# Optimization experiments

Measured on AMD Instinct MI355X. Metric: run time of the kernel, lower is better.

The kernel has to match this reference:

```python
import jax, jax.numpy as jnp
import numpy as np

N = 100000
E = 1600000
DIM_H = 128
NUM_HEADS = 8
HEAD_DIM = DIM_H // NUM_HEADS


def setup_inputs() -> dict:
    key = jax.random.key(0)
    ks = jax.random.split(key, 8)
    s = 1.0 / np.sqrt(DIM_H)
    return {
        "q": jax.random.normal(ks[0], (N, DIM_H), dtype=jnp.float32),
        "kv": jax.random.normal(ks[1], (N, DIM_H), dtype=jnp.float32),
        "edge_index": jax.random.randint(ks[2], (2, E), 0, N, dtype=jnp.int32),
        "W_k": jax.random.normal(ks[3], (DIM_H, DIM_H), dtype=jnp.float32) * s,
        "b_k": jnp.zeros((DIM_H,), dtype=jnp.float32),
        "W_v": jax.random.normal(ks[4], (DIM_H, DIM_H), dtype=jnp.float32) * s,
        "b_v": jnp.zeros((DIM_H,), dtype=jnp.float32),
        "W_o": jax.random.normal(ks[5], (DIM_H, DIM_H), dtype=jnp.float32) * s,
        "b_o": jnp.zeros((DIM_H,), dtype=jnp.float32),
    }


def reference(q, kv, edge_index, W_k, b_k, W_v, b_v, W_o, b_o):
    src, dst = edge_index[0], edge_index[1]
    # Projections: torch Linear is x @ W.T + b
    K = (kv @ W_k.T + b_k).reshape(N, NUM_HEADS, HEAD_DIM)
    V = (kv @ W_v.T + b_v).reshape(N, NUM_HEADS, HEAD_DIM)
    Q = q.reshape(N, NUM_HEADS, HEAD_DIM)

    # Edge-wise attention scores: [E, H]
    scores = jnp.sum(K[src] * Q[dst], axis=-1) / np.sqrt(HEAD_DIM)

    # Sparse softmax over incoming edges of each destination node
    seg_max = jax.ops.segment_max(scores, dst, num_segments=N)  # [N, H]
    ex = jnp.exp(scores - seg_max[dst])
    seg_sum = jax.ops.segment_sum(ex, dst, num_segments=N)  # [N, H]
    attn = ex / (seg_sum[dst] + 1e-16)  # [E, H]

    # Weighted message aggregation (dropout p=0.0 in eval -> identity)
    messages = V[src] * attn[:, :, None]  # [E, H, Hd]
    out = jax.ops.segment_sum(messages, dst, num_segments=N)  # [N, H, Hd]
    out = out.reshape(N, DIM_H)
    return out @ W_o.T + b_o
```

## Files before the change

### kernel.cpp

```cpp
#include <hip/hip_runtime.h>
#include <hip/hip_bf16.h>

#define N_NODES 100000
#define N_EDGES 1600000
#define DIM 128
#define NHEAD 8
#define HDIM 16

#define BSHIFT 9
#define BSZ 512
#define NB 196
#define S1_EDGES 4096

typedef __attribute__((ext_vector_type(8))) short short8;
typedef __attribute__((ext_vector_type(4))) float f32x4;

__device__ __forceinline__ unsigned short f2bf(float f) {
  union { __hip_bfloat16 h; unsigned short u; } c;
  c.h = __float2bfloat16(f);
  return c.u;
}

__global__ __launch_bounds__(256) void cvt3_kernel(const float* __restrict__ a,
                                                   const float* __restrict__ b,
                                                   const float* __restrict__ c,
                                                   unsigned short* __restrict__ y) {
  int i = blockIdx.x * 256 + threadIdx.x;
  const float* src = (i < 4096) ? a : ((i < 8192) ? b : c);
  int j = (i < 4096) ? i : ((i < 8192) ? i - 4096 : i - 8192);
  float4 v = ((const float4*)src)[j];
  ushort4 o;
  o.x = f2bf(v.x); o.y = f2bf(v.y); o.z = f2bf(v.z); o.w = f2bf(v.w);
  ((ushort4*)y)[i] = o;
}


__global__ __launch_bounds__(512) void bhist_kernel(const int* __restrict__ dst,
                                                    int* __restrict__ bcnt) {
  __shared__ int cnt[NB];
  int t = threadIdx.x;
  int base = blockIdx.x * S1_EDGES;
  if (t < NB) cnt[t] = 0;
  __syncthreads();
#pragma unroll
  for (int j = 0; j < S1_EDGES / 512; j++) {
    int e = base + j * 512 + t;
    if (e < N_EDGES) atomicAdd(&cnt[dst[e] >> BSHIFT], 1);
  }
  __syncthreads();
  if (t < NB) {
    int c = cnt[t];
    if (c) atomicAdd(&bcnt[t], c);
  }
}

__global__ __launch_bounds__(256) void bscan_kernel(const int* __restrict__ bcnt,
                                                    int* __restrict__ binBase,
                                                    int* __restrict__ binNext) {
  __shared__ int s[256];
  int t = threadIdx.x;
  int v = (t < NB) ? bcnt[t] : 0;
  s[t] = v;
  __syncthreads();
  for (int off = 1; off < 256; off <<= 1) {
    int x = (t >= off) ? s[t - off] : 0;
    __syncthreads();
    s[t] += x;
    __syncthreads();
  }
  int excl = (t == 0) ? 0 : s[t - 1];
  if (t <= NB) binBase[t] = excl;
  if (t < NB) binNext[t] = excl;
}

__global__ __launch_bounds__(512) void bin_kernel(const int* __restrict__ src,
                                                  const int* __restrict__ dst,
                                                  int* __restrict__ binNext,
                                                  unsigned* __restrict__ binned) {
  __shared__ unsigned pk[S1_EDGES];
  __shared__ unsigned char bkt[S1_EDGES];
  __shared__ int cnt[NB], gb[NB], ln[NB];
  int t = threadIdx.x;
  int base = blockIdx.x * S1_EDGES;
  if (t < NB) { cnt[t] = 0; ln[t] = 0; }
  __syncthreads();
#pragma unroll
  for (int j = 0; j < S1_EDGES / 512; j++) {
    int idx = j * 512 + t;
    int e = base + idx;
    if (e < N_EDGES) {
      int s = src[e], d = dst[e];
      int bb = d >> BSHIFT;
      pk[idx] = (unsigned)s | ((unsigned)(d & (BSZ - 1)) << 17);
      bkt[idx] = (unsigned char)bb;
      atomicAdd(&cnt[bb], 1);
    } else {
      bkt[idx] = 0xFF;
    }
  }
  __syncthreads();
  if (t < NB) {
    int c = cnt[t];
    gb[t] = c ? atomicAdd(&binNext[t], c) : 0;
  }
  __syncthreads();
#pragma unroll
  for (int j = 0; j < S1_EDGES / 512; j++) {
    int idx = j * 512 + t;
    int bb = bkt[idx];
    if (bb != 0xFF) {
      int r = atomicAdd(&ln[bb], 1);
      binned[gb[bb] + r] = pk[idx];
    }
  }
}

__global__ __launch_bounds__(512) void fine_kernel(const unsigned* __restrict__ binned,
                                                   const int* __restrict__ binBase,
                                                   int* __restrict__ rowptr,
                                                   int* __restrict__ esrc) {
  __shared__ int cnt[BSZ], sc[BSZ], nxt[BSZ];
  int b = blockIdx.x, t = threadIdx.x;
  int beg = binBase[b], end = binBase[b + 1];
  cnt[t] = 0;
  __syncthreads();
  for (int i = beg + t; i < end; i += 512) atomicAdd(&cnt[binned[i] >> 17], 1);
  __syncthreads();
  int v = cnt[t];
  sc[t] = v;
  __syncthreads();
  for (int off = 1; off < 512; off <<= 1) {
    int x = (t >= off) ? sc[t - off] : 0;
    __syncthreads();
    sc[t] += x;
    __syncthreads();
  }
  int pos = beg + sc[t] - v;
  int node = b * BSZ + t;
  if (node <= N_NODES) rowptr[node] = pos;
  nxt[t] = pos;
  __syncthreads();
  for (int i = beg + t; i < end; i += 512) {
    unsigned p = binned[i];
    int r = atomicAdd(&nxt[p >> 17], 1);
    esrc[r] = (int)(p & 0x1FFFFu);
  }
}

__global__ __launch_bounds__(256) void kv_proj_mfma(const float* __restrict__ A,
                                                    const unsigned short* __restrict__ Wk,
                                                    const float* __restrict__ bk,
                                                    const unsigned short* __restrict__ Wv,
                                                    const float* __restrict__ bv,
                                                    unsigned short* __restrict__ KV, int n) {
  int w = threadIdx.x >> 6, lane = threadIdx.x & 63;
  int m = lane & 15, quad = lane >> 4;
  int rbase = blockIdx.x * 64 + w * 16;
  int arow = rbase + m;
  if (arow >= n) arow = n - 1;
  const float* ap = A + (size_t)arow * DIM + quad * 8;
  short8 af[4];
#pragma unroll
  for (int t = 0; t < 4; t++) {
    float4 lo = *(const float4*)(ap + 32 * t);
    float4 hi = *(const float4*)(ap + 32 * t + 4);
    short8 f;
    f[0] = (short)f2bf(lo.x); f[1] = (short)f2bf(lo.y);
    f[2] = (short)f2bf(lo.z); f[3] = (short)f2bf(lo.w);
    f[4] = (short)f2bf(hi.x); f[5] = (short)f2bf(hi.y);
    f[6] = (short)f2bf(hi.z); f[7] = (short)f2bf(hi.w);
    af[t] = f;
  }
#pragma unroll
  for (int ct = 0; ct < 16; ct++) {
    const unsigned short* W = (ct < 8) ? Wk : Wv;
    const float* bias = (ct < 8) ? bk : bv;
    int c0 = (ct & 7) * 16;
    const unsigned short* wp = W + (size_t)(c0 + m) * DIM + quad * 8;
    f32x4 acc = {0.f, 0.f, 0.f, 0.f};
    acc = __builtin_amdgcn_mfma_f32_16x16x32_bf16(af[0], *(const short8*)(wp), acc, 0, 0, 0);
    acc = __builtin_amdgcn_mfma_f32_16x16x32_bf16(af[1], *(const short8*)(wp + 32), acc, 0, 0, 0);
    acc = __builtin_amdgcn_mfma_f32_16x16x32_bf16(af[2], *(const short8*)(wp + 64), acc, 0, 0, 0);
    acc = __builtin_amdgcn_mfma_f32_16x16x32_bf16(af[3], *(const short8*)(wp + 96), acc, 0, 0, 0);
    float bb = bias[c0 + m];
    int c = c0 + m;
    int slot = ((ct < 8) ? 0 : 2) + 4 * (c >> 1) + (c & 1);
#pragma unroll
    for (int r = 0; r < 4; r++) {
      int rr = rbase + quad * 4 + r;
      if (rr < n) KV[(size_t)rr * 256 + slot] = f2bf(acc[r] + bb);
    }
  }
}

__global__ __launch_bounds__(256) void o_proj_mfma(const unsigned short* __restrict__ A,
                                                   const unsigned short* __restrict__ Wo,
                                                   const float* __restrict__ bo,
                                                   float* __restrict__ out, int n) {
  int w = threadIdx.x >> 6, lane = threadIdx.x & 63;
  int m = lane & 15, quad = lane >> 4;
  int rbase = blockIdx.x * 64 + w * 16;
  int arow = rbase + m;
  if (arow >= n) arow = n - 1;
  const unsigned short* ap = A + (size_t)arow * DIM + quad * 8;
  short8 af0 = *(const short8*)(ap);
  short8 af1 = *(const short8*)(ap + 32);
  short8 af2 = *(const short8*)(ap + 64);
  short8 af3 = *(const short8*)(ap + 96);
#pragma unroll
  for (int ct = 0; ct < 8; ct++) {
    int c0 = ct * 16;
    const unsigned short* wp = Wo + (size_t)(c0 + m) * DIM + quad * 8;
    f32x4 acc = {0.f, 0.f, 0.f, 0.f};
    acc = __builtin_amdgcn_mfma_f32_16x16x32_bf16(af0, *(const short8*)(wp), acc, 0, 0, 0);
    acc = __builtin_amdgcn_mfma_f32_16x16x32_bf16(af1, *(const short8*)(wp + 32), acc, 0, 0, 0);
    acc = __builtin_amdgcn_mfma_f32_16x16x32_bf16(af2, *(const short8*)(wp + 64), acc, 0, 0, 0);
    acc = __builtin_amdgcn_mfma_f32_16x16x32_bf16(af3, *(const short8*)(wp + 96), acc, 0, 0, 0);
    float bb = bo[c0 + m];
#pragma unroll
    for (int r = 0; r < 4; r++) {
      int rr = rbase + quad * 4 + r;
      if (rr < n) out[(size_t)rr * DIM + c0 + m] = acc[r] + bb;
    }
  }
}

__global__ __launch_bounds__(256) void attn_kernel(const float* __restrict__ q,
                                                   const unsigned short* __restrict__ KV,
                                                   const int* __restrict__ rowptr,
                                                   const int* __restrict__ esrc,
                                                   unsigned short* __restrict__ pre) {
  int wid = blockIdx.x * 4 + __builtin_amdgcn_readfirstlane(threadIdx.x >> 6);
  int lane = threadIdx.x & 63;
  const float SCALE = 0.25f * 1.44269504088896340736f;
  float2 qv = *(const float2*)(q + (size_t)wid * DIM + lane * 2);
  float qx = qv.x * SCALE, qy = qv.y * SCALE;
  const unsigned short* base = KV + lane * 4;

  float l = 0.f, o0 = 0.f, o1 = 0.f;
  int beg = rowptr[wid], end = rowptr[wid + 1];

#define EDGE(d)                                                              \
  {                                                                          \
    float k0 = __uint_as_float((d).x << 16);                                 \
    float k1 = __uint_as_float((d).x & 0xffff0000u);                         \
    float part = fmaf(k1, qy, k0 * qx);                                      \
    part += __shfl_xor(part, 1);                                             \
    part += __shfl_xor(part, 2);                                             \
    part += __shfl_xor(part, 4);                                             \
    float e = exp2f(part);                                                   \
    l += e;                                                                  \
    o0 = fmaf(e, __uint_as_float((d).y << 16), o0);                          \
    o1 = fmaf(e, __uint_as_float((d).y & 0xffff0000u), o1);                  \
  }

  int i = beg;
  for (; i + 4 <= end; i += 4) {
    int s0 = esrc[i + 0], s1 = esrc[i + 1], s2 = esrc[i + 2], s3 = esrc[i + 3];
    uint2 d0 = *(const uint2*)(base + (size_t)s0 * 256);
    uint2 d1 = *(const uint2*)(base + (size_t)s1 * 256);
    uint2 d2 = *(const uint2*)(base + (size_t)s2 * 256);
    uint2 d3 = *(const uint2*)(base + (size_t)s3 * 256);
    EDGE(d0) EDGE(d1) EDGE(d2) EDGE(d3)
  }
  for (; i < end; ++i) {
    int s = esrc[i];
    uint2 d = *(const uint2*)(base + (size_t)s * 256);
    EDGE(d)
  }
#undef EDGE

  float inv = __builtin_amdgcn_rcpf(l + 1e-16f);
  ushort2 r;
  r.x = f2bf(o0 * inv);
  r.y = f2bf(o1 * inv);
  *(ushort2*)(pre + (size_t)wid * DIM + lane * 2) = r;
}


extern "C" void kernel_launch(void* const* d_in, const int* in_sizes, int n_in,
                              void* d_out, int out_size, void* d_ws, size_t ws_size,
                              hipStream_t stream) {
  const float* q  = (const float*)d_in[0];
  const float* kv = (const float*)d_in[1];
  const int* ei   = (const int*)d_in[2];
  const float* Wk = (const float*)d_in[3];
  const float* bk = (const float*)d_in[4];
  const float* Wv = (const float*)d_in[5];
  const float* bv = (const float*)d_in[6];
  const float* Wo = (const float*)d_in[7];
  const float* bo = (const float*)d_in[8];
  float* out = (float*)d_out;
  const int* srcp = ei;
  const int* dstp = ei + N_EDGES;

  char* ws = (char*)d_ws;
  size_t o = 0;
  auto alloc = [&](size_t bytes) {
    void* p = ws + o;
    o += (bytes + 511) & ~(size_t)511;
    return p;
  };
  unsigned short* Wkb = (unsigned short*)alloc((size_t)DIM * DIM * 2);
  unsigned short* Wvb = (unsigned short*)alloc((size_t)DIM * DIM * 2);
  unsigned short* Wob = (unsigned short*)alloc((size_t)DIM * DIM * 2);
  unsigned short* KV  = (unsigned short*)alloc((size_t)N_NODES * 256 * 2);
  unsigned short* pre = (unsigned short*)alloc((size_t)N_NODES * DIM * 2);
  int* esrc      = (int*)alloc((size_t)N_EDGES * 4);
  unsigned* binned = (unsigned*)alloc((size_t)N_EDGES * 4);
  int* rowptr    = (int*)alloc((size_t)(N_NODES + 1) * 4);
  int* bcnt      = (int*)alloc((size_t)NB * 4);
  int* binBase   = (int*)alloc((size_t)(NB + 1) * 4);
  int* binNext   = (int*)alloc((size_t)NB * 4);
  (void)ws_size;

  hipMemsetAsync(bcnt, 0, (size_t)NB * 4, stream);
  cvt3_kernel<<<48, 256, 0, stream>>>(Wk, Wv, Wo, Wkb);
  int nbblk = (N_EDGES + S1_EDGES - 1) / S1_EDGES;
  bhist_kernel<<<nbblk, 512, 0, stream>>>(dstp, bcnt);
  bscan_kernel<<<1, 256, 0, stream>>>(bcnt, binBase, binNext);
  bin_kernel<<<nbblk, 512, 0, stream>>>(srcp, dstp, binNext, binned);
  fine_kernel<<<NB, 512, 0, stream>>>(binned, binBase, rowptr, esrc);
  kv_proj_mfma<<<(N_NODES + 63) / 64, 256, 0, stream>>>(kv, Wkb, bk, Wvb, bv, KV, N_NODES);
  attn_kernel<<<N_NODES / 4, 256, 0, stream>>>(q, KV, rowptr, esrc, pre);
  o_proj_mfma<<<(N_NODES + 63) / 64, 256, 0, stream>>>(pre, Wob, bo, out, N_NODES);
}
```

Baseline: 400.3 us.

## Process two edges per wavefront with 16-byte KV gathers and LDS-staged KV stores

The KV row layout changes to interleave 4 K and 4 V bf16 values per 16-byte chunk. The attention kernel now splits each wavefront into two halves that handle alternate edges, with each lane gathering one uint4. Partial sums are combined with a cross-half shuffle at the end, and an odd trailing edge is masked with a zero weight. The projection kernel stages outputs in shared memory and writes full coalesced 16-byte rows instead of scattered 2-byte stores. The aim is fewer, wider gather transactions and better store coalescing, at the cost of extra LDS use and a final reduction.

```diff
diff --git a/kernel.cpp b/kernel.cpp
--- a/kernel.cpp
+++ b/kernel.cpp
@@ -153,6 +153,7 @@
                                                     const unsigned short* __restrict__ Wv,
                                                     const float* __restrict__ bv,
                                                     unsigned short* __restrict__ KV, int n) {
+  __shared__ unsigned short tile[64][264];
   int w = threadIdx.x >> 6, lane = threadIdx.x & 63;
   int m = lane & 15, quad = lane >> 4;
   int rbase = blockIdx.x * 64 + w * 16;
@@ -184,12 +185,20 @@
     acc = __builtin_amdgcn_mfma_f32_16x16x32_bf16(af[3], *(const short8*)(wp + 96), acc, 0, 0, 0);
     float bb = bias[c0 + m];
     int c = c0 + m;
-    int slot = ((ct < 8) ? 0 : 2) + 4 * (c >> 1) + (c & 1);
-#pragma unroll
-    for (int r = 0; r < 4; r++) {
-      int rr = rbase + quad * 4 + r;
-      if (rr < n) KV[(size_t)rr * 256 + slot] = f2bf(acc[r] + bb);
-    }
+    int pos = ((ct < 8) ? 0 : 4) + (c >> 2) * 8 + (c & 3);
+    int lr = w * 16 + quad * 4;
+#pragma unroll
+    for (int r = 0; r < 4; r++) tile[lr + r][pos] = f2bf(acc[r] + bb);
+  }
+  __syncthreads();
+#pragma unroll
+  for (int it = 0; it < 8; it++) {
+    int cidx = it * 256 + threadIdx.x;
+    int row = cidx >> 5;
+    int off = (cidx & 31) * 8;
+    int g = blockIdx.x * 64 + row;
+    if (g < n)
+      *(uint4*)(KV + (size_t)g * 256 + off) = *(const uint4*)(&tile[row][off]);
   }
 }
 
@@ -232,49 +241,76 @@
                                                    unsigned short* __restrict__ pre) {
   int wid = blockIdx.x * 4 + __builtin_amdgcn_readfirstlane(threadIdx.x >> 6);
   int lane = threadIdx.x & 63;
+  int half = lane >> 5;
+  int p = lane & 31;
   const float SCALE = 0.25f * 1.44269504088896340736f;
-  float2 qv = *(const float2*)(q + (size_t)wid * DIM + lane * 2);
-  float qx = qv.x * SCALE, qy = qv.y * SCALE;
-  const unsigned short* base = KV + lane * 4;
-
-  float l = 0.f, o0 = 0.f, o1 = 0.f;
+  float4 qv = *(const float4*)(q + (size_t)wid * DIM + p * 4);
+  float qx = qv.x * SCALE, qy = qv.y * SCALE, qz = qv.z * SCALE, qw = qv.w * SCALE;
+  const unsigned short* base = KV + p * 8;
+
+  float l = 0.f, o0 = 0.f, o1 = 0.f, o2 = 0.f, o3 = 0.f;
   int beg = rowptr[wid], end = rowptr[wid + 1];
 
-#define EDGE(d)                                                              \
+#define EDGE2(d, wgt)                                                        \
   {                                                                          \
     float k0 = __uint_as_float((d).x << 16);                                 \
     float k1 = __uint_as_float((d).x & 0xffff0000u);                         \
+    float k2 = __uint_as_float((d).y << 16);                                 \
+    float k3 = __uint_as_float((d).y & 0xffff0000u);                         \
     float part = fmaf(k1, qy, k0 * qx);                                      \
+    part = fmaf(k3, qw, fmaf(k2, qz, part));                                 \
     part += __shfl_xor(part, 1);                                             \
     part += __shfl_xor(part, 2);                                             \
-    part += __shfl_xor(part, 4);                                             \
-    float e = exp2f(part);                                                   \
+    float e = exp2f(part) * (wgt);                                           \
     l += e;                                                                  \
-    o0 = fmaf(e, __uint_as_float((d).y << 16), o0);                          \
-    o1 = fmaf(e, __uint_as_float((d).y & 0xffff0000u), o1);                  \
+    o0 = fmaf(e, __uint_as_float((d).z << 16), o0);                          \
+    o1 = fmaf(e, __uint_as_float((d).z & 0xffff0000u), o1);                  \
+    o2 = fmaf(e, __uint_as_float((d).w << 16), o2);                          \
+    o3 = fmaf(e, __uint_as_float((d).w & 0xffff0000u), o3);                  \
   }
 
   int i = beg;
-  for (; i + 4 <= end; i += 4) {
-    int s0 = esrc[i + 0], s1 = esrc[i + 1], s2 = esrc[i + 2], s3 = esrc[i + 3];
-    uint2 d0 = *(const uint2*)(base + (size_t)s0 * 256);
-    uint2 d1 = *(const uint2*)(base + (size_t)s1 * 256);
-    uint2 d2 = *(const uint2*)(base + (size_t)s2 * 256);
-    uint2 d3 = *(const uint2*)(base + (size_t)s3 * 256);
-    EDGE(d0) EDGE(d1) EDGE(d2) EDGE(d3)
-  }
-  for (; i < end; ++i) {
+  for (; i + 8 <= end; i += 8) {
+    int4 sa = *(const int4*)(esrc + i);
+    int4 sb = *(const int4*)(esrc + i + 4);
+    int s0 = half ? sa.y : sa.x;
+    int s1 = half ? sa.w : sa.z;
+    int s2 = half ? sb.y : sb.x;
+    int s3 = half ? sb.w : sb.z;
+    uint4 d0 = *(const uint4*)(base + (size_t)s0 * 256);
+    uint4 d1 = *(const uint4*)(base + (size_t)s1 * 256);
+    uint4 d2 = *(const uint4*)(base + (size_t)s2 * 256);
+    uint4 d3 = *(const uint4*)(base + (size_t)s3 * 256);
+    EDGE2(d0, 1.f) EDGE2(d1, 1.f) EDGE2(d2, 1.f) EDGE2(d3, 1.f)
+  }
+  for (; i + 2 <= end; i += 2) {
+    int s = esrc[i + half];
+    uint4 d = *(const uint4*)(base + (size_t)s * 256);
+    EDGE2(d, 1.f)
+  }
+  if (i < end) {
     int s = esrc[i];
-    uint2 d = *(const uint2*)(base + (size_t)s * 256);
-    EDGE(d)
-  }
-#undef EDGE
+    uint4 d = *(const uint4*)(base + (size_t)s * 256);
+    float hm = half ? 0.f : 1.f;
+    EDGE2(d, hm)
+  }
+#undef EDGE2
+
+  l += __shfl_xor(l, 32);
+  o0 += __shfl_xor(o0, 32);
+  o1 += __shfl_xor(o1, 32);
+  o2 += __shfl_xor(o2, 32);
+  o3 += __shfl_xor(o3, 32);
 
   float inv = __builtin_amdgcn_rcpf(l + 1e-16f);
-  ushort2 r;
-  r.x = f2bf(o0 * inv);
-  r.y = f2bf(o1 * inv);
-  *(ushort2*)(pre + (size_t)wid * DIM + lane * 2) = r;
+  if (half == 0) {
+    ushort4 r;
+    r.x = f2bf(o0 * inv);
+    r.y = f2bf(o1 * inv);
+    r.z = f2bf(o2 * inv);
+    r.w = f2bf(o3 * inv);
+    *(ushort4*)(pre + (size_t)wid * DIM + p * 4) = r;
+  }
 }
 
 
```

New measurement: 386.6 us. 3.4% less time.
